# Kernel tuning notes

Measured on AMD Instinct MI355X. Metric: run time of the kernel, lower is better.

## Reference

```python
import jax, jax.numpy as jnp
import numpy as np

B, Lq, Lkv = 4, 1024, 4096
Cq, Ckv, E, NH = 512, 512, 512, 8
HD = E // NH


def setup_inputs() -> dict:
    key = jax.random.key(0)
    ks = jax.random.split(key, 8)
    s = 0.02
    return {
        "Xq": jax.random.normal(ks[0], (B, Lq, Cq), dtype=jnp.float32),
        "Xkv": jax.random.normal(ks[1], (B, Lkv, Ckv), dtype=jnp.float32),
        "mask": jax.random.randint(ks[2], (B, Lq, 1), 0, 2, dtype=jnp.int32),
        "Wq": jax.random.normal(ks[3], (Cq, E), dtype=jnp.float32) * s,
        "bq": jnp.zeros((E,), dtype=jnp.float32),
        "Wkv": jax.random.normal(ks[4], (Ckv, 2 * E), dtype=jnp.float32) * s,
        "bkv": jnp.zeros((2 * E,), dtype=jnp.float32),
        "Wp": jax.random.normal(ks[5], (E, E), dtype=jnp.float32) * s,
        "bp": jnp.zeros((E,), dtype=jnp.float32),
        "attn_pos": jax.random.normal(ks[6], (1, NH, Lq, Lkv), dtype=jnp.float32) * s,
    }


def reference(Xq, Xkv, mask, Wq, bq, Wkv, bkv, Wp, bp, attn_pos):
    scale = HD ** -0.5
    # projections
    Q = (Xq @ Wq + bq).reshape(B, Lq, NH, HD).transpose(0, 2, 1, 3) * scale  # [B,NH,Lq,HD]
    KV = (Xkv @ Wkv + bkv).reshape(B, Lkv, 2, NH, HD)
    K = KV[:, :, 0].transpose(0, 2, 1, 3)  # [B,NH,Lkv,HD]
    V = KV[:, :, 1].transpose(0, 2, 1, 3)
    # scores + learned positional bias
    attn = jnp.einsum('bhqd,bhkd->bhqk', Q, K) + attn_pos  # [B,NH,Lq,Lkv]
    # dummy-column masked softmax (mask: [B,Lq,1], 1=keep row)
    m = mask.astype(attn.dtype)[:, None]           # [B,1,Lq,1]
    attn = attn + (1.0 - m) * (-100.0)             # suppress masked query rows
    dummy = jnp.broadcast_to(jnp.where(m == 0, 100.0, -100.0), (B, NH, Lq, 1))
    attn = jax.nn.softmax(jnp.concatenate([attn, dummy], axis=-1), axis=-1)[..., :Lkv]
    # weighted sum + output projection (dropout = identity in eval)
    out = jnp.einsum('bhqk,bhkd->bhqd', attn, V)
    out = out.transpose(0, 2, 1, 3).reshape(B, Lq, E)
    return out @ Wp + bp
```

## Files before the change

kernel.cpp:

```cpp
#include <hip/hip_runtime.h>

typedef unsigned short u16;
typedef __attribute__((ext_vector_type(8))) short bf16x8;
typedef __attribute__((ext_vector_type(4))) float f32x4;
typedef __attribute__((ext_vector_type(2))) unsigned u32x2;
typedef __attribute__((ext_vector_type(4))) unsigned u32x4;

__device__ __forceinline__ u16 f2bf(float x) {
    union { float f; unsigned u; } v; v.f = x;
    unsigned r = v.u + 0x7FFF + ((v.u >> 16) & 1);
    return (u16)(r >> 16);
}

__device__ __forceinline__ unsigned cvt_pk_bf16(float lo, float hi) {
    unsigned r;
    asm("v_cvt_pk_bf16_f32 %0, %1, %2" : "=v"(r) : "v"(lo), "v"(hi));
    return r;
}

__device__ __forceinline__ bf16x8 pk8(const f32x4& s0, const f32x4& s1) {
    union { u32x4 u; bf16x8 v; } x;
    x.u[0] = cvt_pk_bf16(s0[0], s0[1]);
    x.u[1] = cvt_pk_bf16(s0[2], s0[3]);
    x.u[2] = cvt_pk_bf16(s1[0], s1[1]);
    x.u[3] = cvt_pk_bf16(s1[2], s1[3]);
    return x.v;
}

__device__ __forceinline__ void gl_lds16(const u16* g, u16* l) {
    __builtin_amdgcn_global_load_lds((const __attribute__((address_space(1))) void*)g,
                                     (__attribute__((address_space(3))) void*)l, 16, 0, 0);
}

__global__ __launch_bounds__(256) void conv_bf16_2(const float* __restrict__ Xq,
                                                   const float* __restrict__ Xkv,
                                                   u16* __restrict__ oq,
                                                   u16* __restrict__ okv) {
    int bid = blockIdx.x;
    const float* in;
    u16* out;
    size_t i;
    if (bid < 1024) {
        in = Xq; out = oq;
        i = ((size_t)bid * 256 + threadIdx.x) * 8;
    } else {
        in = Xkv; out = okv;
        i = ((size_t)(bid - 1024) * 256 + threadIdx.x) * 8;
    }
    const float4* p = (const float4*)(in + i);
    float4 a = p[0], b = p[1];
    u32x4 w = {cvt_pk_bf16(a.x, a.y), cvt_pk_bf16(a.z, a.w),
               cvt_pk_bf16(b.x, b.y), cvt_pk_bf16(b.z, b.w)};
    *(u32x4*)(out + i) = w;
}

__global__ __launch_bounds__(256) void transpose_w3(const float* __restrict__ Wq,
                                                    const float* __restrict__ Wkv,
                                                    const float* __restrict__ Wp,
                                                    u16* __restrict__ WqT,
                                                    u16* __restrict__ WkvT,
                                                    u16* __restrict__ WpT) {
    __shared__ float tile[64][65];
    int bid = blockIdx.x;
    const float* in;
    u16* out;
    int R = 512, C, bx, by;
    if (bid < 64) {
        in = Wq; out = WqT; C = 512; bx = bid & 7; by = bid >> 3;
    } else if (bid < 192) {
        bid -= 64;
        in = Wkv; out = WkvT; C = 1024; bx = bid & 15; by = bid >> 4;
    } else {
        bid -= 192;
        in = Wp; out = WpT; C = 512; bx = bid & 7; by = bid >> 3;
    }
    int r0 = by * 64, c0 = bx * 64;
    int tid = threadIdx.x;
#pragma unroll
    for (int j = 0; j < 16; ++j) {
        int e = tid + j * 256;
        int row = e >> 6, col = e & 63;
        tile[row][col] = in[(size_t)(r0 + row) * C + c0 + col];
    }
    __syncthreads();
#pragma unroll
    for (int j = 0; j < 16; ++j) {
        int e = tid + j * 256;
        int row = e >> 6, col = e & 63;
        out[(size_t)(c0 + row) * R + r0 + col] = f2bf(tile[col][row]);
    }
}

template <int MODE>
__global__ __launch_bounds__(256) void gemm_kernel(const u16* __restrict__ A,
                                                   const u16* __restrict__ Bt,
                                                   const float* __restrict__ bias,
                                                   void* __restrict__ Cout,
                                                   void* __restrict__ Cout2,
                                                   int M, int N, int K) {
    __shared__ u16 Al[128][64];
    __shared__ u16 Bl[128][64];
    int tid = threadIdx.x;
    int lane = tid & 63, wid = tid >> 6;
    int wr = wid >> 1, wc = wid & 1;
    int l15 = lane & 15, g = lane >> 4;
    int bm = blockIdx.y, bn = blockIdx.x;
    int ldr = lane >> 3, ldc = (lane & 7) << 3;

    f32x4 acc[4][4];
#pragma unroll
    for (int m = 0; m < 4; ++m)
#pragma unroll
        for (int n = 0; n < 4; ++n)
#pragma unroll
            for (int j = 0; j < 4; ++j) acc[m][n][j] = 0.f;

    int nK = K >> 6;
    for (int kt = 0; kt < nK; ++kt) {
        __syncthreads();
#pragma unroll
        for (int i = 0; i < 4; ++i) {
            int c = wid * 4 + i;
            int row = c * 8 + ldr;
            gl_lds16(A + (size_t)(bm * 128 + row) * K + kt * 64 + ldc, &Al[0][0] + c * 512);
            gl_lds16(Bt + (size_t)(bn * 128 + row) * K + kt * 64 + ldc, &Bl[0][0] + c * 512);
        }
        __syncthreads();

#pragma unroll
        for (int kk = 0; kk < 2; ++kk) {
            bf16x8 af[4], bfr[4];
#pragma unroll
            for (int m = 0; m < 4; ++m)
                af[m] = *(const bf16x8*)&Al[wr * 64 + m * 16 + l15][kk * 32 + g * 8];
#pragma unroll
            for (int n = 0; n < 4; ++n)
                bfr[n] = *(const bf16x8*)&Bl[wc * 64 + n * 16 + l15][kk * 32 + g * 8];
#pragma unroll
            for (int m = 0; m < 4; ++m)
#pragma unroll
                for (int n = 0; n < 4; ++n)
                    acc[m][n] =
                        __builtin_amdgcn_mfma_f32_16x16x32_bf16(af[m], bfr[n], acc[m][n], 0, 0, 0);
        }
    }

#pragma unroll
    for (int m = 0; m < 4; ++m)
#pragma unroll
        for (int n = 0; n < 4; ++n)
#pragma unroll
            for (int j = 0; j < 4; ++j) {
                int row = bm * 128 + wr * 64 + m * 16 + g * 4 + j;
                int col = bn * 128 + wc * 64 + n * 16 + l15;
                float v = acc[m][n][j] + bias[col];
                if (MODE == 1) {
                    int b = row >> 12, kv = row & 4095;
                    if (col < 512) {
                        int h = col >> 6, d = col & 63;
                        ((u16*)Cout)[(((size_t)((b * 8 + h) * 4096 + kv)) << 6) + d] = f2bf(v);
                    } else {
                        int c2 = col - 512;
                        int h = c2 >> 6, d = c2 & 63;
                        int p = j | ((m & 1) << 2) | (g << 3);
                        int dkv = (kv & ~31) | p;
                        ((u16*)Cout2)[((size_t)(b * 8 + h) * 64 + d) * 4096 + dkv] = f2bf(v);
                    }
                } else {
                    ((float*)Cout)[(size_t)row * N + col] = v;
                }
            }
}

template <int MODE>
__global__ __launch_bounds__(256) void gemm_n64(const u16* __restrict__ A,
                                                const u16* __restrict__ Bt,
                                                const float* __restrict__ bias,
                                                void* __restrict__ Cout,
                                                int M, int N, int K) {
    __shared__ u16 Al[128][64];
    __shared__ u16 Bl[64][64];
    int tid = threadIdx.x;
    int lane = tid & 63, wid = tid >> 6;
    int wr = wid >> 1, wc = wid & 1;
    int l15 = lane & 15, g = lane >> 4;
    int bm = blockIdx.y, bn = blockIdx.x;
    int ldr = lane >> 3, ldc = (lane & 7) << 3;

    f32x4 acc[4][2];
#pragma unroll
    for (int m = 0; m < 4; ++m)
#pragma unroll
        for (int n = 0; n < 2; ++n)
#pragma unroll
            for (int j = 0; j < 4; ++j) acc[m][n][j] = 0.f;

    int nK = K >> 6;
    for (int kt = 0; kt < nK; ++kt) {
        __syncthreads();
#pragma unroll
        for (int i = 0; i < 6; ++i) {
            int c = wid * 6 + i;
            if (c < 16) {
                int row = c * 8 + ldr;
                gl_lds16(A + (size_t)(bm * 128 + row) * K + kt * 64 + ldc, &Al[0][0] + c * 512);
            } else {
                int cb = c - 16;
                int row = cb * 8 + ldr;
                gl_lds16(Bt + (size_t)(bn * 64 + row) * K + kt * 64 + ldc, &Bl[0][0] + cb * 512);
            }
        }
        __syncthreads();

#pragma unroll
        for (int kk = 0; kk < 2; ++kk) {
            bf16x8 af[4], bfr[2];
#pragma unroll
            for (int m = 0; m < 4; ++m)
                af[m] = *(const bf16x8*)&Al[wr * 64 + m * 16 + l15][kk * 32 + g * 8];
#pragma unroll
            for (int n = 0; n < 2; ++n)
                bfr[n] = *(const bf16x8*)&Bl[wc * 32 + n * 16 + l15][kk * 32 + g * 8];
#pragma unroll
            for (int m = 0; m < 4; ++m)
#pragma unroll
                for (int n = 0; n < 2; ++n)
                    acc[m][n] =
                        __builtin_amdgcn_mfma_f32_16x16x32_bf16(af[m], bfr[n], acc[m][n], 0, 0, 0);
        }
    }

#pragma unroll
    for (int m = 0; m < 4; ++m)
#pragma unroll
        for (int n = 0; n < 2; ++n)
#pragma unroll
            for (int j = 0; j < 4; ++j) {
                int row = bm * 128 + wr * 64 + m * 16 + g * 4 + j;
                int col = bn * 64 + wc * 32 + n * 16 + l15;
                float v = acc[m][n][j] + bias[col];
                if (MODE == 0) {
                    int b = row >> 10, q = row & 1023, h = col >> 6, d = col & 63;
                    ((u16*)Cout)[(((size_t)((b * 8 + h) * 1024 + q)) << 6) + d] =
                        f2bf(v * 0.18033688011112042f);
                } else {
                    ((float*)Cout)[(size_t)row * N + col] = v;
                }
            }
}

__global__ __launch_bounds__(256, 2) void attn_kernel(const u16* __restrict__ Qb,
                                                      const u16* __restrict__ Kb,
                                                      const u16* __restrict__ Vt,
                                                      const float* __restrict__ pos,
                                                      float* __restrict__ Opart,
                                                      float* __restrict__ Lp) {
    __shared__ u16 Klds[4][4096];
    __shared__ u16 Vlds[4][4096];

    int idx = blockIdx.x;
    int h = idx & 7;
    int rest = idx >> 3;
    int qt = rest & 15, sp = rest >> 4;
    int q0 = qt * 64;
    int kvbase = sp * 1024;
    int tid = threadIdx.x, lane = tid & 63, wid = tid >> 6;
    int l15 = lane & 15, g = lane >> 4;

    bf16x8 aq[4][2];
#pragma unroll
    for (int b = 0; b < 4; ++b) {
        const u16* qp =
            Qb + (((size_t)((b * 8 + h) * 1024 + q0 + wid * 16 + l15)) << 6) + g * 8;
        aq[b][0] = *(const bf16x8*)(qp);
        aq[b][1] = *(const bf16x8*)(qp + 32);
    }

    f32x4 o[4][4];
    f32x4 lacc[4];
#pragma unroll
    for (int b = 0; b < 4; ++b) {
#pragma unroll
        for (int j = 0; j < 4; ++j) lacc[b][j] = 0.f;
#pragma unroll
        for (int n = 0; n < 4; ++n)
#pragma unroll
            for (int j = 0; j < 4; ++j) o[b][n][j] = 0.f;
    }

    const u16* Kg = Kb + ((size_t)(wid * 8 + h)) * 4096 * 64;
    const u16* Vg = Vt + ((size_t)(wid * 8 + h)) * 4096 * 64;
    u16* KldsW = &Klds[wid][0];
    u16* VldsW = &Vlds[wid][0];
    int lr = lane >> 3;
    int lcs = ((lane & 7) ^ lr) << 3;

    const float* posq =
        pos + (size_t)h * 1024 * 4096 + (size_t)(q0 + wid * 16 + l15) * 4096 + kvbase;

    const short one_s = (short)0x3F80;
    bf16x8 ones = {one_s, one_s, one_s, one_s, one_s, one_s, one_s, one_s};
    int sw = (l15 & 7) << 4;

    f32x4 zr[4];
    for (int kt = 0; kt < 16; ++kt) {
        int kv0 = kvbase + kt * 64;
        __syncthreads();
#pragma unroll
        for (int c = 0; c < 8; ++c)
            gl_lds16(Kg + (size_t)(kv0 + c * 8 + lr) * 64 + lcs, KldsW + c * 512);
#pragma unroll
        for (int c = 0; c < 8; ++c)
            gl_lds16(Vg + (size_t)(c * 8 + lr) * 4096 + kv0 + lcs, VldsW + c * 512);
#pragma unroll
        for (int n = 0; n < 4; ++n) {
            zr[n] = *(const f32x4*)(posq + kt * 64 + n * 16 + g * 4);
#pragma unroll
            for (int j = 0; j < 4; ++j) zr[n][j] *= 1.44269504f;
        }
        __syncthreads();

#pragma unroll
        for (int b = 0; b < 4; ++b) {
            const char* KbL = (const char*)&Klds[b][0];
            const char* VbL = (const char*)&Vlds[b][0];

            f32x4 s[4];
            __builtin_amdgcn_s_setprio(1);
#pragma unroll
            for (int n = 0; n < 4; ++n) {
                bf16x8 kb0 = *(const bf16x8*)(KbL + (n * 16 + l15) * 128 + ((g * 16) ^ sw));
                bf16x8 kb1 = *(const bf16x8*)(KbL + (n * 16 + l15) * 128 + ((64 + g * 16) ^ sw));
                f32x4 t = __builtin_amdgcn_mfma_f32_16x16x32_bf16(kb0, aq[b][0], zr[n], 0, 0, 0);
                s[n] = __builtin_amdgcn_mfma_f32_16x16x32_bf16(kb1, aq[b][1], t, 0, 0, 0);
            }
            __builtin_amdgcn_s_setprio(0);

#pragma unroll
            for (int n = 0; n < 4; ++n)
#pragma unroll
                for (int j = 0; j < 4; ++j) s[n][j] = __builtin_exp2f(s[n][j]);

            bf16x8 pa0 = pk8(s[0], s[1]);
            bf16x8 pa1 = pk8(s[2], s[3]);

            __builtin_amdgcn_s_setprio(1);
#pragma unroll
            for (int n = 0; n < 4; ++n) {
                bf16x8 vb0 = *(const bf16x8*)(VbL + (n * 16 + l15) * 128 + ((g * 16) ^ sw));
                bf16x8 vb1 = *(const bf16x8*)(VbL + (n * 16 + l15) * 128 + ((64 + g * 16) ^ sw));
                o[b][n] = __builtin_amdgcn_mfma_f32_16x16x32_bf16(pa0, vb0, o[b][n], 0, 0, 0);
                o[b][n] = __builtin_amdgcn_mfma_f32_16x16x32_bf16(pa1, vb1, o[b][n], 0, 0, 0);
            }
            lacc[b] = __builtin_amdgcn_mfma_f32_16x16x32_bf16(pa0, ones, lacc[b], 0, 0, 0);
            lacc[b] = __builtin_amdgcn_mfma_f32_16x16x32_bf16(pa1, ones, lacc[b], 0, 0, 0);
            __builtin_amdgcn_s_setprio(0);
        }
    }

#pragma unroll
    for (int b = 0; b < 4; ++b) {
        int obase = (sp * 32 + b * 8 + h) * 1024;
#pragma unroll
        for (int j = 0; j < 4; ++j) {
            int row = q0 + wid * 16 + g * 4 + j;
#pragma unroll
            for (int n = 0; n < 4; ++n)
                __builtin_nontemporal_store(o[b][n][j],
                                            &Opart[((size_t)(obase + row)) * 64 + n * 16 + l15]);
            if (l15 == 0) __builtin_nontemporal_store(lacc[b][j], &Lp[obase + row]);
        }
    }
}

__global__ __launch_bounds__(256) void attn_combine(const float* __restrict__ Opart,
                                                    const float* __restrict__ Lp,
                                                    const int* __restrict__ mask,
                                                    u16* __restrict__ AO) {
    int tid = threadIdx.x;
    int d = tid & 63;
    int r = blockIdx.x * 4 + (tid >> 6);
    int bh = r >> 10, q = r & 1023;
    int b = bh >> 3, h = bh & 7;

    float L = 0.f, val = 0.f;
#pragma unroll
    for (int s2 = 0; s2 < 4; ++s2) {
        size_t rr = (size_t)(s2 * 32 + bh) * 1024 + q;
        L += Lp[rr];
        val += Opart[rr * 64 + d];
    }
    float res = mask[b * 1024 + q] ? (val / L) : 0.f;
    AO[((size_t)(b * 1024 + q)) * 512 + h * 64 + d] = f2bf(res);
}

extern "C" void kernel_launch(void* const* d_in, const int* in_sizes, int n_in,
                              void* d_out, int out_size, void* d_ws, size_t ws_size,
                              hipStream_t stream) {
    const float* Xq = (const float*)d_in[0];
    const float* Xkv = (const float*)d_in[1];
    const int* mask = (const int*)d_in[2];
    const float* Wq = (const float*)d_in[3];
    const float* bq = (const float*)d_in[4];
    const float* Wkv = (const float*)d_in[5];
    const float* bkv = (const float*)d_in[6];
    const float* Wp = (const float*)d_in[7];
    const float* bp = (const float*)d_in[8];
    const float* pos = (const float*)d_in[9];
    float* out = (float*)d_out;

    char* ws = (char*)d_ws;
    u16* WqT = (u16*)(ws);
    u16* WkvT = (u16*)(ws + 524288);
    u16* WpT = (u16*)(ws + 1572864);
    u16* Qb = (u16*)(ws + 2097152);
    u16* Kb = (u16*)(ws + 6291456);
    u16* Vt = (u16*)(ws + 23068672);
    u16* AO = (u16*)(ws + 39845888);
    float* Opart = (float*)(ws + 44040192);
    u16* Xkvb = (u16*)(ws + 44040192);
    u16* Xqb = (u16*)(ws + 60817408);
    float* Lp = (float*)(ws + 111149056);

    conv_bf16_2<<<dim3(5120), 256, 0, stream>>>(Xq, Xkv, Xqb, Xkvb);
    transpose_w3<<<dim3(256), 256, 0, stream>>>(Wq, Wkv, Wp, WqT, WkvT, WpT);
    gemm_n64<0><<<dim3(8, 32), 256, 0, stream>>>(Xqb, WqT, bq, Qb, 4096, 512, 512);
    gemm_kernel<1><<<dim3(8, 128), 256, 0, stream>>>(Xkvb, WkvT, bkv, Kb, Vt, 16384, 1024, 512);
    attn_kernel<<<dim3(512), 256, 0, stream>>>(Qb, Kb, Vt, pos, Opart, Lp);
    attn_combine<<<dim3(8192), 256, 0, stream>>>(Opart, Lp, mask, AO);
    gemm_n64<2><<<dim3(8, 32), 256, 0, stream>>>(AO, WpT, bp, out, 4096, 512, 512);
}
```

Before: 182.0 us.

## Double-buffer K/V LDS tiles with 32-wide KV steps and prefetch

Splits each 64-key tile into 32-key steps and keeps two LDS buffers, so the next step's K/V global-to-LDS loads and positional-bias reads are issued before the current step's MFMA work. This removes one barrier per iteration and lets memory traffic overlap with compute. The V tile layout and swizzle are reworked so the smaller tile fits. The cost is twice as many loop iterations with less MFMA work in each, and the same total LDS footprint.

```diff
diff --git a/kernel.cpp b/kernel.cpp
--- a/kernel.cpp
+++ b/kernel.cpp
@@ -255,8 +255,8 @@
                                                       const float* __restrict__ pos,
                                                       float* __restrict__ Opart,
                                                       float* __restrict__ Lp) {
-    __shared__ u16 Klds[4][4096];
-    __shared__ u16 Vlds[4][4096];
+    __shared__ u16 Klds[2][4][2048];
+    __shared__ u16 Vlds[2][4][2048];
 
     int idx = blockIdx.x;
     int h = idx & 7;
@@ -290,10 +290,10 @@
 
     const u16* Kg = Kb + ((size_t)(wid * 8 + h)) * 4096 * 64;
     const u16* Vg = Vt + ((size_t)(wid * 8 + h)) * 4096 * 64;
-    u16* KldsW = &Klds[wid][0];
-    u16* VldsW = &Vlds[wid][0];
     int lr = lane >> 3;
     int lcs = ((lane & 7) ^ lr) << 3;
+    int vhalf = (lane >> 2) & 1;
+    int vslot = (lane & 3) ^ (lr & 3);
 
     const float* posq =
         pos + (size_t)h * 1024 * 4096 + (size_t)(q0 + wid * 16 + l15) * 4096 + kvbase;
@@ -302,33 +302,46 @@
     bf16x8 ones = {one_s, one_s, one_s, one_s, one_s, one_s, one_s, one_s};
     int sw = (l15 & 7) << 4;
 
-    f32x4 zr[4];
-    for (int kt = 0; kt < 16; ++kt) {
-        int kv0 = kvbase + kt * 64;
+    auto STAGE = [&](int buf, int t) {
+        int kv0 = kvbase + t * 32;
+#pragma unroll
+        for (int c = 0; c < 4; ++c) {
+            gl_lds16(Kg + (size_t)(kv0 + c * 8 + lr) * 64 + lcs, &Klds[buf][wid][c * 512]);
+            gl_lds16(Vg + (size_t)(2 * (c * 8 + lr) + vhalf) * 4096 + kv0 + vslot * 8,
+                     &Vlds[buf][wid][c * 512]);
+        }
+    };
+
+    STAGE(0, 0);
+    f32x4 zr[2];
+#pragma unroll
+    for (int n = 0; n < 2; ++n) {
+        zr[n] = *(const f32x4*)(posq + n * 16 + g * 4);
+#pragma unroll
+        for (int j = 0; j < 4; ++j) zr[n][j] *= 1.44269504f;
+    }
+
+    for (int kt = 0; kt < 32; ++kt) {
+        int cur = kt & 1;
         __syncthreads();
-#pragma unroll
-        for (int c = 0; c < 8; ++c)
-            gl_lds16(Kg + (size_t)(kv0 + c * 8 + lr) * 64 + lcs, KldsW + c * 512);
-#pragma unroll
-        for (int c = 0; c < 8; ++c)
-            gl_lds16(Vg + (size_t)(c * 8 + lr) * 4096 + kv0 + lcs, VldsW + c * 512);
-#pragma unroll
-        for (int n = 0; n < 4; ++n) {
-            zr[n] = *(const f32x4*)(posq + kt * 64 + n * 16 + g * 4);
-#pragma unroll
-            for (int j = 0; j < 4; ++j) zr[n][j] *= 1.44269504f;
-        }
-        __syncthreads();
+
+        f32x4 zn0, zn1;
+        if (kt < 31) {
+            zn0 = *(const f32x4*)(posq + (kt + 1) * 32 + g * 4);
+            zn1 = *(const f32x4*)(posq + (kt + 1) * 32 + 16 + g * 4);
+            __builtin_amdgcn_sched_barrier(0);
+            STAGE(cur ^ 1, kt + 1);
+        }
 
 #pragma unroll
         for (int b = 0; b < 4; ++b) {
-            const char* KbL = (const char*)&Klds[b][0];
-            const char* VbL = (const char*)&Vlds[b][0];
-
-            f32x4 s[4];
+            const char* KbL = (const char*)&Klds[cur][b][0];
+            const char* VbL = (const char*)&Vlds[cur][b][0];
+
+            f32x4 s[2];
             __builtin_amdgcn_s_setprio(1);
 #pragma unroll
-            for (int n = 0; n < 4; ++n) {
+            for (int n = 0; n < 2; ++n) {
                 bf16x8 kb0 = *(const bf16x8*)(KbL + (n * 16 + l15) * 128 + ((g * 16) ^ sw));
                 bf16x8 kb1 = *(const bf16x8*)(KbL + (n * 16 + l15) * 128 + ((64 + g * 16) ^ sw));
                 f32x4 t = __builtin_amdgcn_mfma_f32_16x16x32_bf16(kb0, aq[b][0], zr[n], 0, 0, 0);
@@ -337,24 +350,31 @@
             __builtin_amdgcn_s_setprio(0);
 
 #pragma unroll
-            for (int n = 0; n < 4; ++n)
+            for (int n = 0; n < 2; ++n)
 #pragma unroll
                 for (int j = 0; j < 4; ++j) s[n][j] = __builtin_exp2f(s[n][j]);
 
-            bf16x8 pa0 = pk8(s[0], s[1]);
-            bf16x8 pa1 = pk8(s[2], s[3]);
+            bf16x8 pa = pk8(s[0], s[1]);
 
             __builtin_amdgcn_s_setprio(1);
 #pragma unroll
             for (int n = 0; n < 4; ++n) {
-                bf16x8 vb0 = *(const bf16x8*)(VbL + (n * 16 + l15) * 128 + ((g * 16) ^ sw));
-                bf16x8 vb1 = *(const bf16x8*)(VbL + (n * 16 + l15) * 128 + ((64 + g * 16) ^ sw));
-                o[b][n] = __builtin_amdgcn_mfma_f32_16x16x32_bf16(pa0, vb0, o[b][n], 0, 0, 0);
-                o[b][n] = __builtin_amdgcn_mfma_f32_16x16x32_bf16(pa1, vb1, o[b][n], 0, 0, 0);
-            }
-            lacc[b] = __builtin_amdgcn_mfma_f32_16x16x32_bf16(pa0, ones, lacc[b], 0, 0, 0);
-            lacc[b] = __builtin_amdgcn_mfma_f32_16x16x32_bf16(pa1, ones, lacc[b], 0, 0, 0);
+                int vd = n * 16 + l15;
+                int vr = vd >> 1;
+                int vbyte = (vr << 7) + ((vd & 1) << 6) + (((g ^ (vr & 3)) & 3) << 4);
+                bf16x8 vb = *(const bf16x8*)(VbL + vbyte);
+                o[b][n] = __builtin_amdgcn_mfma_f32_16x16x32_bf16(pa, vb, o[b][n], 0, 0, 0);
+            }
+            lacc[b] = __builtin_amdgcn_mfma_f32_16x16x32_bf16(pa, ones, lacc[b], 0, 0, 0);
             __builtin_amdgcn_s_setprio(0);
+        }
+
+        if (kt < 31) {
+#pragma unroll
+            for (int j = 0; j < 4; ++j) {
+                zr[0][j] = zn0[j] * 1.44269504f;
+                zr[1][j] = zn1[j] * 1.44269504f;
+            }
         }
     }
 
```

Result: slower. 190.8 us (+4.8%).
